# Optimization experiments

Measured on AMD Instinct MI355X. Metric: run time of the kernel, lower is better.

Reference implementation:

```python
import jax, jax.numpy as jnp
import numpy as np

N_NODES = 50000
N_EDGES = 800000
N_GRAPHS = 64
D_IN = 128
DIMS = (256, 256)


def _glorot(key, shape):
    fan_in, fan_out = shape[0], shape[1]
    lim = jnp.sqrt(6.0 / (fan_in + fan_out)).astype(jnp.float32)
    return jax.random.uniform(key, shape, jnp.float32, -lim, lim)


def setup_inputs() -> dict:
    key = jax.random.key(0)
    ks = jax.random.split(key, 12)
    x = jax.random.normal(ks[0], (N_NODES, D_IN), dtype=jnp.float32)
    edge_index = jax.random.randint(ks[1], (2, N_EDGES), 0, N_NODES, dtype=jnp.int64)
    batch = jnp.sort(jax.random.randint(ks[2], (N_NODES,), 0, N_GRAPHS, dtype=jnp.int64))
    # MLP params per GIN layer: Linear(in,dim) -> ReLU -> Linear(dim,dim) -> ReLU
    W1_0 = _glorot(ks[3], (D_IN, DIMS[0]))
    b1_0 = jnp.zeros((DIMS[0],), jnp.float32)
    W2_0 = _glorot(ks[4], (DIMS[0], DIMS[0]))
    b2_0 = jnp.zeros((DIMS[0],), jnp.float32)
    W1_1 = _glorot(ks[5], (DIMS[0], DIMS[1]))
    b1_1 = jnp.zeros((DIMS[1],), jnp.float32)
    W2_1 = _glorot(ks[6], (DIMS[1], DIMS[1]))
    b2_1 = jnp.zeros((DIMS[1],), jnp.float32)
    return {"x": x, "edge_index": edge_index, "batch": batch,
            "W1_0": W1_0, "b1_0": b1_0, "W2_0": W2_0, "b2_0": b2_0,
            "W1_1": W1_1, "b1_1": b1_1, "W2_1": W2_1, "b2_1": b2_1}


def _gin_layer(x, src, dst, W1, b1, W2, b2):
    # aggregate: sum of neighbor features (messages from src into dst)
    agg = jax.ops.segment_sum(x[src], dst, num_segments=N_NODES)
    h = x + agg  # (1 + eps) * x + agg, eps = 0
    h = jax.nn.relu(h @ W1 + b1)
    h = jax.nn.relu(h @ W2 + b2)
    return h


def reference(x, edge_index, batch, W1_0, b1_0, W2_0, b2_0, W1_1, b1_1, W2_1, b2_1):
    src, dst = edge_index[0], edge_index[1]
    h = _gin_layer(x, src, dst, W1_0, b1_0, W2_0, b2_0)
    h = _gin_layer(h, src, dst, W1_1, b1_1, W2_1, b2_1)
    # global mean pool over graphs
    sums = jax.ops.segment_sum(h, batch, num_segments=N_GRAPHS)
    counts = jax.ops.segment_sum(jnp.ones((h.shape[0],), h.dtype), batch, num_segments=N_GRAPHS)
    return sums / jnp.maximum(counts, 1.0)[:, None]
```

## Files before the change

### kernel.cpp

```cpp
#include <hip/hip_runtime.h>


typedef __bf16 bf16x8 __attribute__((ext_vector_type(8)));
typedef float f32x4 __attribute__((ext_vector_type(4)));

#define N_NODES 50000
#define N_EDGES 800000
#define N_GRAPHS 64
#define SCAN_BLOCKS 196
#define NREP 8

#define PB_HIST0 3125
#define PB_P0    6250
#define PB_P1    6378
#define PB_P2    6634
#define PB_P3    6890
#define PB_BIAS  7146
#define PB_TOTAL 7150

#define OFF_FLAGS  0ull
#define OFF_WB     64ull
#define OFF_WP0    4096ull
#define OFF_WP1    (OFF_WP0 + 65536ull)
#define OFF_WP2    (OFF_WP1 + 131072ull)
#define OFF_WP3    (OFF_WP2 + 131072ull)
#define OFF_CNT    462848ull
#define OFF_ROWPTR 662864ull
#define OFF_CURSOR 862880ull
#define OFF_SSRC   1062912ull
#define OFF_A      2662912ull
#define OFF_B      15462912ull
#define OFF_C      41062912ull
#define OFF_POOL32 66662912ull
#define OFF_BSUM   67187200ull
#define OFF_DCNT   67189248ull
#define OFF_DCUR   67190272ull
#define OFF_PERM   67191296ull

__device__ __forceinline__ float b2f(unsigned short u) {
  union { unsigned int i; float f; } v; v.i = ((unsigned int)u) << 16; return v.f;
}
__device__ __forceinline__ float b2f_lo(unsigned int u) {
  union { unsigned int i; float f; } v; v.i = u << 16; return v.f;
}
__device__ __forceinline__ float b2f_hi(unsigned int u) {
  union { unsigned int i; float f; } v; v.i = u & 0xffff0000u; return v.f;
}
__device__ __forceinline__ unsigned short f2b(float f) {
  union { unsigned int i; float f; } v; v.f = f;
  unsigned int r = v.i + 0x7fffu + ((v.i >> 16) & 1u);
  return (unsigned short)(r >> 16);
}
__device__ __forceinline__ unsigned int pk2(float hi, float lo) {
  return ((unsigned int)f2b(hi) << 16) | f2b(lo);
}
__device__ __forceinline__ void acc8(float* a, uint4 v) {
  a[0] += b2f_lo(v.x); a[1] += b2f_hi(v.x);
  a[2] += b2f_lo(v.y); a[3] += b2f_hi(v.y);
  a[4] += b2f_lo(v.z); a[5] += b2f_hi(v.z);
  a[6] += b2f_lo(v.w); a[7] += b2f_hi(v.w);
}

__global__ void detect_zero(const unsigned int* __restrict__ xw,
                            const unsigned int* __restrict__ eiw,
                            int* __restrict__ flags,
                            int* __restrict__ counts, float* __restrict__ pool32,
                            int* __restrict__ dcnt, int* __restrict__ dcur) {
  if (blockIdx.x == 0) {
    __shared__ int s_f[256], s_i[256];
    int t = threadIdx.x;
    int fh = 0, iz = 0;
    for (int i = t; i < 1024; i += 256) {
      unsigned int e = (xw[i] >> 7) & 0xFFu;
      fh += (e >= 115u && e <= 130u) ? 1 : 0;
      iz += (eiw[2 * i + 1] == 0u) ? 1 : 0;
    }
    s_f[t] = fh; s_i[t] = iz;
    __syncthreads();
    for (int s = 128; s > 0; s >>= 1) {
      if (t < s) { s_f[t] += s_f[t + s]; s_i[t] += s_i[t + s]; }
      __syncthreads();
    }
    if (t == 0) { flags[0] = s_f[0] > 512 ? 1 : 0; flags[1] = s_i[0] > 512 ? 1 : 0; }
  } else {
    int i = (blockIdx.x - 1) * 256 + threadIdx.x;
    if (i < N_NODES) counts[i] = 0;
    if (i < NREP * N_GRAPHS * 256) pool32[i] = 0.f;
    if (i < 256) { dcnt[i] = 0; dcur[i] = 0; }
  }
}

__device__ __forceinline__ void pack_w_elem(const void* W, unsigned short* Wp,
                                            int e, int isb) {
  int n = e & 255;
  int krow = e >> 8;
  int kb = krow >> 5, r = krow & 31;
  int q = r >> 3, j = r & 7;
  size_t out = ((((size_t)(kb << 8) + n) << 2) + q) * 8 + j;
  Wp[out] = isb ? ((const unsigned short*)W)[e] : f2b(((const float*)W)[e]);
}

__global__ void prep_kernel(const void* __restrict__ x, const int* __restrict__ ei,
                            const void* W0, const void* W1, const void* W2, const void* W3,
                            const void* b0, const void* b1, const void* b2, const void* b3,
                            unsigned short* __restrict__ A,
                            int* __restrict__ counts,
                            unsigned short* __restrict__ Wp0, unsigned short* __restrict__ Wp1,
                            unsigned short* __restrict__ Wp2, unsigned short* __restrict__ Wp3,
                            unsigned short* __restrict__ Wb,
                            const int* __restrict__ flags) {
  int b = blockIdx.x, t = threadIdx.x;
  int isb = flags[0];
  if (b < PB_HIST0) {
    if (!isb) {
      int i = b * 256 + t;
      const float4* f = (const float4*)x;
      float4 a = f[2 * i], c = f[2 * i + 1];
      ushort4 o0; o0.x = f2b(a.x); o0.y = f2b(a.y); o0.z = f2b(a.z); o0.w = f2b(a.w);
      ushort4 o1; o1.x = f2b(c.x); o1.y = f2b(c.y); o1.z = f2b(c.z); o1.w = f2b(c.w);
      ((ushort4*)A)[2 * i] = o0;
      ((ushort4*)A)[2 * i + 1] = o1;
    }
  } else if (b < PB_P0) {
    int e = (b - PB_HIST0) * 256 + t;
    int dst = flags[1] ? ei[2 * (N_EDGES + e)] : ei[N_EDGES + e];
    atomicAdd(&counts[dst], 1);
  } else if (b < PB_P1) {
    pack_w_elem(W0, Wp0, (b - PB_P0) * 256 + t, isb);
  } else if (b < PB_P2) {
    pack_w_elem(W1, Wp1, (b - PB_P1) * 256 + t, isb);
  } else if (b < PB_P3) {
    pack_w_elem(W2, Wp2, (b - PB_P2) * 256 + t, isb);
  } else if (b < PB_BIAS) {
    pack_w_elem(W3, Wp3, (b - PB_P3) * 256 + t, isb);
  } else {
    int i = (b - PB_BIAS) * 256 + t;
    const void* p = (i < 256) ? b0 : (i < 512) ? b1 : (i < 768) ? b2 : b3;
    int n = i & 255;
    Wb[i] = isb ? ((const unsigned short*)p)[n] : f2b(((const float*)p)[n]);
  }
}

__global__ void scan_blocks(const int* __restrict__ counts,
                            int* __restrict__ rowptr, int* __restrict__ bsum,
                            int* __restrict__ dcnt) {
  __shared__ int sd[256], lh[256];
  int t = threadIdx.x;
  int i = blockIdx.x * 256 + t;
  int v = (i < N_NODES) ? counts[i] : 0;
  sd[t] = v;
  lh[t] = 0;
  __syncthreads();
  if (i < N_NODES) atomicAdd(&lh[v > 255 ? 255 : v], 1);
  __syncthreads();
  if (lh[t] > 0) atomicAdd(&dcnt[t], lh[t]);
  for (int off = 1; off < 256; off <<= 1) {
    int u = (t >= off) ? sd[t - off] : 0;
    __syncthreads();
    sd[t] += u;
    __syncthreads();
  }
  if (i < N_NODES) rowptr[i] = sd[t] - v;
  if (t == 255) bsum[blockIdx.x] = sd[255];
}

__global__ void scan_fix(int* __restrict__ rowptr, int* __restrict__ cursor,
                         const int* __restrict__ bsum, const int* __restrict__ counts,
                         const int* __restrict__ dcnt, int* __restrict__ dcur,
                         int* __restrict__ perm) {
  __shared__ int sb[256], db[256], base[256], lc[256];
  int t = threadIdx.x;
  sb[t] = (t < SCAN_BLOCKS) ? bsum[t] : 0;
  db[t] = dcnt[t];
  lc[t] = 0;
  __syncthreads();
  for (int off = 1; off < 256; off <<= 1) {
    int u1 = (t >= off) ? sb[t - off] : 0;
    int u2 = (t >= off) ? db[t - off] : 0;
    __syncthreads();
    sb[t] += u1; db[t] += u2;
    __syncthreads();
  }
  db[t] -= dcnt[t];
  __syncthreads();
  int boffv = (blockIdx.x > 0) ? sb[blockIdx.x - 1] : 0;
  int i = blockIdx.x * 256 + t;
  int d = 0;
  if (i < N_NODES) {
    int v = rowptr[i] + boffv;
    rowptr[i] = v;
    cursor[i] = v;
    int c = counts[i];
    d = c > 255 ? 255 : c;
    atomicAdd(&lc[d], 1);
  }
  if (i == 0) rowptr[N_NODES] = N_EDGES;
  __syncthreads();
  int cnt = lc[t];
  base[t] = (cnt > 0) ? (db[t] + atomicAdd(&dcur[t], cnt)) : 0;
  __syncthreads();
  lc[t] = 0;
  __syncthreads();
  if (i < N_NODES) {
    int r = atomicAdd(&lc[d], 1);
    perm[base[d] + r] = i;
  }
}

__global__ void fill_kernel(const int* __restrict__ ei, int* __restrict__ cursor,
                            unsigned short* __restrict__ ssrc,
                            const int* __restrict__ flags) {
  int e = blockIdx.x * blockDim.x + threadIdx.x;
  if (e >= N_EDGES) return;
  int is64 = flags[1];
  int src = is64 ? ei[2 * e] : ei[e];
  int dst = is64 ? ei[2 * (N_EDGES + e)] : ei[N_EDGES + e];
  int pos = atomicAdd(&cursor[dst], 1);
  ssrc[pos] = (unsigned short)src;
}

__global__ void fused_gather_gemm(const unsigned short* __restrict__ featCanon,
                                  const unsigned short* __restrict__ featRaw,
                                  const int* __restrict__ rowptr,
                                  const unsigned short* __restrict__ ssrc,
                                  const int* __restrict__ perm,
                                  const unsigned short* __restrict__ Wp,
                                  const unsigned short* __restrict__ Wb, int bias_row,
                                  unsigned short* __restrict__ C, int D,
                                  const int* __restrict__ flags) {
  __shared__ __align__(16) unsigned short Alds[16 * 264];
  __shared__ int sp[16];
  const int S = D + 8;
  const int row0 = blockIdx.x << 4;
  const int lane = threadIdx.x & 63;
  const int wave = threadIdx.x >> 6;
  const unsigned short* feat = flags[0] ? featRaw : featCanon;
  if (threadIdx.x < 16) sp[threadIdx.x] = perm[row0 + threadIdx.x];
  __syncthreads();

  {
    int sub = lane >> 4;
    int l = lane & 15;
    int nl = (wave << 2) + sub;
    int node = sp[nl];
    int beg = rowptr[node], end = rowptr[node + 1];
    int c = l << 3;
    if (D == 256) {
      float a[16];
#pragma unroll
      for (int j = 0; j < 16; ++j) a[j] = 0.f;
      const unsigned short* spt = feat + (size_t)node * 256 + c;
      acc8(a, *(const uint4*)spt);
      acc8(a + 8, *(const uint4*)(spt + 128));
      int i = beg;
      for (; i + 3 < end; i += 4) {
        int ss[4];
#pragma unroll
        for (int e = 0; e < 4; ++e) ss[e] = ssrc[i + e];
        uint4 v[8];
#pragma unroll
        for (int e = 0; e < 4; ++e) {
          const unsigned short* p = feat + (size_t)ss[e] * 256 + c;
          v[2 * e] = *(const uint4*)p;
          v[2 * e + 1] = *(const uint4*)(p + 128);
        }
#pragma unroll
        for (int e = 0; e < 4; ++e) { acc8(a, v[2 * e]); acc8(a + 8, v[2 * e + 1]); }
      }
      for (; i < end; ++i) {
        const unsigned short* p = feat + (size_t)ssrc[i] * 256 + c;
        acc8(a, *(const uint4*)p);
        acc8(a + 8, *(const uint4*)(p + 128));
      }
      uint4 o0, o1;
      o0.x = pk2(a[1], a[0]);  o0.y = pk2(a[3], a[2]);
      o0.z = pk2(a[5], a[4]);  o0.w = pk2(a[7], a[6]);
      o1.x = pk2(a[9], a[8]);  o1.y = pk2(a[11], a[10]);
      o1.z = pk2(a[13], a[12]); o1.w = pk2(a[15], a[14]);
      *(uint4*)(&Alds[nl * S + c]) = o0;
      *(uint4*)(&Alds[nl * S + c + 128]) = o1;
    } else {
      float a[8];
#pragma unroll
      for (int j = 0; j < 8; ++j) a[j] = 0.f;
      acc8(a, *(const uint4*)(feat + (size_t)node * 128 + c));
      int i = beg;
      for (; i + 3 < end; i += 4) {
        int ss[4];
#pragma unroll
        for (int e = 0; e < 4; ++e) ss[e] = ssrc[i + e];
        uint4 v[4];
#pragma unroll
        for (int e = 0; e < 4; ++e)
          v[e] = *(const uint4*)(feat + (size_t)ss[e] * 128 + c);
#pragma unroll
        for (int e = 0; e < 4; ++e) acc8(a, v[e]);
      }
      for (; i < end; ++i)
        acc8(a, *(const uint4*)(feat + (size_t)ssrc[i] * 128 + c));
      uint4 o0;
      o0.x = pk2(a[1], a[0]); o0.y = pk2(a[3], a[2]);
      o0.z = pk2(a[5], a[4]); o0.w = pk2(a[7], a[6]);
      *(uint4*)(&Alds[nl * S + c]) = o0;
    }
  }
  __syncthreads();

  const int m = lane & 15;
  const int q = lane >> 4;
  f32x4 acc[4];
#pragma unroll
  for (int t = 0; t < 4; ++t) acc[t] = (f32x4){0.f, 0.f, 0.f, 0.f};

  const unsigned short* arow = &Alds[m * S + (q << 3)];
  const int nb = (wave << 6) + m;
  const int kblocks = D >> 5;
  for (int kb = 0; kb < kblocks; ++kb) {
    bf16x8 af = *(const bf16x8*)(arow + (kb << 5));
    const unsigned short* wp = Wp + (((size_t)(kb << 8) + nb) * 4 + q) * 8;
    bf16x8 b0 = *(const bf16x8*)(wp);
    bf16x8 b1 = *(const bf16x8*)(wp + 512);
    bf16x8 b2 = *(const bf16x8*)(wp + 1024);
    bf16x8 b3 = *(const bf16x8*)(wp + 1536);
    acc[0] = __builtin_amdgcn_mfma_f32_16x16x32_bf16(af, b0, acc[0], 0, 0, 0);
    acc[1] = __builtin_amdgcn_mfma_f32_16x16x32_bf16(af, b1, acc[1], 0, 0, 0);
    acc[2] = __builtin_amdgcn_mfma_f32_16x16x32_bf16(af, b2, acc[2], 0, 0, 0);
    acc[3] = __builtin_amdgcn_mfma_f32_16x16x32_bf16(af, b3, acc[3], 0, 0, 0);
  }
#pragma unroll
  for (int t = 0; t < 4; ++t) {
    int n = (wave << 6) + (t << 4) + m;
    float bv = b2f(Wb[bias_row * 256 + n]);
#pragma unroll
    for (int i = 0; i < 4; ++i) {
      int r = sp[(q << 2) + i];
      float v = fmaxf(acc[t][i] + bv, 0.f);
      C[(size_t)r * 256 + n] = f2b(v);
    }
  }
}

__global__ void gemm_relu(const unsigned short* __restrict__ A,
                          const unsigned short* __restrict__ Wp,
                          const unsigned short* __restrict__ Wb, int bias_row,
                          unsigned short* __restrict__ C, int K) {
  const int row0 = blockIdx.x << 4;
  const int lane = threadIdx.x & 63;
  const int wave = threadIdx.x >> 6;
  const int m = lane & 15;
  const int q = lane >> 4;
  f32x4 acc[4];
#pragma unroll
  for (int t = 0; t < 4; ++t) acc[t] = (f32x4){0.f, 0.f, 0.f, 0.f};

  const unsigned short* arow = A + (size_t)(row0 + m) * K + (q << 3);
  const int nb = (wave << 6) + m;
  const int kblocks = K >> 5;
  for (int kb = 0; kb < kblocks; ++kb) {
    bf16x8 af = *(const bf16x8*)(arow + (kb << 5));
    const unsigned short* wp = Wp + (((size_t)(kb << 8) + nb) * 4 + q) * 8;
    bf16x8 b0 = *(const bf16x8*)(wp);
    bf16x8 b1 = *(const bf16x8*)(wp + 512);
    bf16x8 b2 = *(const bf16x8*)(wp + 1024);
    bf16x8 b3 = *(const bf16x8*)(wp + 1536);
    acc[0] = __builtin_amdgcn_mfma_f32_16x16x32_bf16(af, b0, acc[0], 0, 0, 0);
    acc[1] = __builtin_amdgcn_mfma_f32_16x16x32_bf16(af, b1, acc[1], 0, 0, 0);
    acc[2] = __builtin_amdgcn_mfma_f32_16x16x32_bf16(af, b2, acc[2], 0, 0, 0);
    acc[3] = __builtin_amdgcn_mfma_f32_16x16x32_bf16(af, b3, acc[3], 0, 0, 0);
  }
#pragma unroll
  for (int t = 0; t < 4; ++t) {
    int n = (wave << 6) + (t << 4) + m;
    float bv = b2f(Wb[bias_row * 256 + n]);
#pragma unroll
    for (int i = 0; i < 4; ++i) {
      int r = row0 + (q << 2) + i;
      float v = fmaxf(acc[t][i] + bv, 0.f);
      C[(size_t)r * 256 + n] = f2b(v);
    }
  }
}

__global__ void gemm_pool(const unsigned short* __restrict__ A,
                          const unsigned short* __restrict__ Wp,
                          const unsigned short* __restrict__ Wb, int bias_row,
                          float* __restrict__ pool32, const int* __restrict__ batch,
                          const int* __restrict__ flags, int K) {
  __shared__ int sg[16];
  const int row0 = blockIdx.x << 4;
  const int lane = threadIdx.x & 63;
  const int wave = threadIdx.x >> 6;
  float* pr = pool32 + ((blockIdx.x & (NREP - 1)) << 14);
  if (threadIdx.x < 16) {
    int r = row0 + threadIdx.x;
    sg[threadIdx.x] = flags[1] ? batch[2 * r] : batch[r];
  }
  __syncthreads();

  const int m = lane & 15;
  const int q = lane >> 4;
  f32x4 acc[4];
#pragma unroll
  for (int t = 0; t < 4; ++t) acc[t] = (f32x4){0.f, 0.f, 0.f, 0.f};

  const unsigned short* arow = A + (size_t)(row0 + m) * K + (q << 3);
  const int nb = (wave << 6) + m;
  const int kblocks = K >> 5;
  for (int kb = 0; kb < kblocks; ++kb) {
    bf16x8 af = *(const bf16x8*)(arow + (kb << 5));
    const unsigned short* wp = Wp + (((size_t)(kb << 8) + nb) * 4 + q) * 8;
    bf16x8 b0 = *(const bf16x8*)(wp);
    bf16x8 b1 = *(const bf16x8*)(wp + 512);
    bf16x8 b2 = *(const bf16x8*)(wp + 1024);
    bf16x8 b3 = *(const bf16x8*)(wp + 1536);
    acc[0] = __builtin_amdgcn_mfma_f32_16x16x32_bf16(af, b0, acc[0], 0, 0, 0);
    acc[1] = __builtin_amdgcn_mfma_f32_16x16x32_bf16(af, b1, acc[1], 0, 0, 0);
    acc[2] = __builtin_amdgcn_mfma_f32_16x16x32_bf16(af, b2, acc[2], 0, 0, 0);
    acc[3] = __builtin_amdgcn_mfma_f32_16x16x32_bf16(af, b3, acc[3], 0, 0, 0);
  }

  int uniform = (sg[0] == sg[15]);
#pragma unroll
  for (int t = 0; t < 4; ++t) {
    int n = (wave << 6) + (t << 4) + m;
    float bv = b2f(Wb[bias_row * 256 + n]);
    float v0 = fmaxf(acc[t][0] + bv, 0.f);
    float v1 = fmaxf(acc[t][1] + bv, 0.f);
    float v2 = fmaxf(acc[t][2] + bv, 0.f);
    float v3 = fmaxf(acc[t][3] + bv, 0.f);
    if (uniform) {
      float ps = v0 + v1 + v2 + v3;
      ps += __shfl_xor(ps, 16);
      ps += __shfl_xor(ps, 32);
      if (q == 0) unsafeAtomicAdd(&pr[sg[0] * 256 + n], ps);
    } else {
      int gp = sg[q << 2];
      float a = 0.f;
      float vv[4] = {v0, v1, v2, v3};
#pragma unroll
      for (int i = 0; i < 4; ++i) {
        int g = sg[(q << 2) + i];
        if (g != gp) { unsafeAtomicAdd(&pr[gp * 256 + n], a); a = 0.f; gp = g; }
        a += vv[i];
      }
      unsafeAtomicAdd(&pr[gp * 256 + n], a);
    }
  }
}

__device__ __forceinline__ int lower_bound(const int* a, int n, int v, int is64) {
  int lo = 0, hi = n;
  while (lo < hi) {
    int mid = (lo + hi) >> 1;
    int bv = is64 ? a[2 * mid] : a[mid];
    if (bv < v) lo = mid + 1; else hi = mid;
  }
  return lo;
}

__global__ void pool_final(const float* __restrict__ pool32,
                           const int* __restrict__ batch,
                           void* __restrict__ out,
                           const int* __restrict__ flags) {
  __shared__ int sh[2];
  int g = blockIdx.x;
  int is64 = flags[1];
  if (threadIdx.x == 0) sh[0] = lower_bound(batch, N_NODES, g, is64);
  if (threadIdx.x == 1) sh[1] = lower_bound(batch, N_NODES, g + 1, is64);
  __syncthreads();
  int c = threadIdx.x;
  float s = 0.f;
#pragma unroll
  for (int r = 0; r < NREP; ++r) s += pool32[(r << 14) + g * 256 + c];
  float res = s / fmaxf((float)(sh[1] - sh[0]), 1.0f);
  if (flags[0]) ((unsigned short*)out)[(size_t)g * 256 + c] = f2b(res);
  else          ((float*)out)[(size_t)g * 256 + c] = res;
}

extern "C" void kernel_launch(void* const* d_in, const int* in_sizes, int n_in,
                              void* d_out, int out_size, void* d_ws, size_t ws_size,
                              hipStream_t stream) {
  const void* x    = d_in[0];
  const int*  ei   = (const int*)d_in[1];
  const int*  batch= (const int*)d_in[2];

  char* ws = (char*)d_ws;
  int*            flags = (int*)(ws + OFF_FLAGS);
  unsigned short* Wb    = (unsigned short*)(ws + OFF_WB);
  unsigned short* Wp0   = (unsigned short*)(ws + OFF_WP0);
  unsigned short* Wp1   = (unsigned short*)(ws + OFF_WP1);
  unsigned short* Wp2   = (unsigned short*)(ws + OFF_WP2);
  unsigned short* Wp3   = (unsigned short*)(ws + OFF_WP3);
  int*            cnts  = (int*)(ws + OFF_CNT);
  int*            rowp  = (int*)(ws + OFF_ROWPTR);
  int*            curs  = (int*)(ws + OFF_CURSOR);
  unsigned short* ssrc  = (unsigned short*)(ws + OFF_SSRC);
  unsigned short* A     = (unsigned short*)(ws + OFF_A);
  unsigned short* B     = (unsigned short*)(ws + OFF_B);
  unsigned short* C     = (unsigned short*)(ws + OFF_C);
  float*          pool32= (float*)(ws + OFF_POOL32);
  int*            bsum  = (int*)(ws + OFF_BSUM);
  int*            dcnt  = (int*)(ws + OFF_DCNT);
  int*            dcur  = (int*)(ws + OFF_DCUR);
  int*            perm  = (int*)(ws + OFF_PERM);

  detect_zero<<<513, 256, 0, stream>>>((const unsigned int*)x, (const unsigned int*)ei,
                                       flags, cnts, pool32, dcnt, dcur);
  prep_kernel<<<PB_TOTAL, 256, 0, stream>>>(x, ei,
                                            d_in[3], d_in[5], d_in[7], d_in[9],
                                            d_in[4], d_in[6], d_in[8], d_in[10],
                                            A, cnts, Wp0, Wp1, Wp2, Wp3, Wb, flags);
  scan_blocks<<<SCAN_BLOCKS, 256, 0, stream>>>(cnts, rowp, bsum, dcnt);
  scan_fix<<<SCAN_BLOCKS, 256, 0, stream>>>(rowp, curs, bsum, cnts, dcnt, dcur, perm);
  fill_kernel<<<3125, 256, 0, stream>>>(ei, curs, ssrc, flags);

  fused_gather_gemm<<<3125, 256, 0, stream>>>(A, (const unsigned short*)x, rowp, ssrc,
                                              perm, Wp0, Wb, 0, C, 128, flags);
  gemm_relu<<<3125, 256, 0, stream>>>(C, Wp1, Wb, 1, B, 256);

  fused_gather_gemm<<<3125, 256, 0, stream>>>(B, B, rowp, ssrc,
                                              perm, Wp2, Wb, 2, C, 256, flags);
  gemm_pool<<<3125, 256, 0, stream>>>(C, Wp3, Wb, 3, pool32, batch, flags, 256);

  pool_final<<<N_GRAPHS, 256, 0, stream>>>(pool32, batch, d_out, flags);
}
```

Measured before the change: 378.2 us.

## Fuse each GIN layer's gather and both MLP GEMMs into one kernel

Each GIN layer now runs in a single kernel: neighbour aggregation, first linear+ReLU kept in shared memory, then second linear+ReLU (and pooling for layer 2). This removes the intermediate C buffer round trip and two launches. Layer 2 uses 512-thread blocks so each wave covers fewer output columns. The degree-sorting permutation is now built per block with a local prefix scan instead of a global histogram, so nodes are sorted by degree only within each 256-node block. That removes global atomics but gives weaker load balancing across blocks.

```diff
diff --git a/kernel.cpp b/kernel.cpp
--- a/kernel.cpp
+++ b/kernel.cpp
@@ -30,11 +30,8 @@
 #define OFF_SSRC   1062912ull
 #define OFF_A      2662912ull
 #define OFF_B      15462912ull
-#define OFF_C      41062912ull
 #define OFF_POOL32 66662912ull
 #define OFF_BSUM   67187200ull
-#define OFF_DCNT   67189248ull
-#define OFF_DCUR   67190272ull
 #define OFF_PERM   67191296ull
 
 __device__ __forceinline__ float b2f(unsigned short u) {
@@ -64,8 +61,7 @@
 __global__ void detect_zero(const unsigned int* __restrict__ xw,
                             const unsigned int* __restrict__ eiw,
                             int* __restrict__ flags,
-                            int* __restrict__ counts, float* __restrict__ pool32,
-                            int* __restrict__ dcnt, int* __restrict__ dcur) {
+                            int* __restrict__ counts, float* __restrict__ pool32) {
   if (blockIdx.x == 0) {
     __shared__ int s_f[256], s_i[256];
     int t = threadIdx.x;
@@ -86,7 +82,6 @@
     int i = (blockIdx.x - 1) * 256 + threadIdx.x;
     if (i < N_NODES) counts[i] = 0;
     if (i < NREP * N_GRAPHS * 256) pool32[i] = 0.f;
-    if (i < 256) { dcnt[i] = 0; dcur[i] = 0; }
   }
 }
 
@@ -142,18 +137,13 @@
 }
 
 __global__ void scan_blocks(const int* __restrict__ counts,
-                            int* __restrict__ rowptr, int* __restrict__ bsum,
-                            int* __restrict__ dcnt) {
-  __shared__ int sd[256], lh[256];
+                            int* __restrict__ rowptr, int* __restrict__ bsum) {
+  __shared__ int sd[256];
   int t = threadIdx.x;
   int i = blockIdx.x * 256 + t;
   int v = (i < N_NODES) ? counts[i] : 0;
   sd[t] = v;
-  lh[t] = 0;
-  __syncthreads();
-  if (i < N_NODES) atomicAdd(&lh[v > 255 ? 255 : v], 1);
-  __syncthreads();
-  if (lh[t] > 0) atomicAdd(&dcnt[t], lh[t]);
+  __syncthreads();
   for (int off = 1; off < 256; off <<= 1) {
     int u = (t >= off) ? sd[t - off] : 0;
     __syncthreads();
@@ -166,44 +156,46 @@
 
 __global__ void scan_fix(int* __restrict__ rowptr, int* __restrict__ cursor,
                          const int* __restrict__ bsum, const int* __restrict__ counts,
-                         const int* __restrict__ dcnt, int* __restrict__ dcur,
                          int* __restrict__ perm) {
-  __shared__ int sb[256], db[256], base[256], lc[256];
+  __shared__ int sb[256], lh[256], lc2[256];
   int t = threadIdx.x;
   sb[t] = (t < SCAN_BLOCKS) ? bsum[t] : 0;
-  db[t] = dcnt[t];
-  lc[t] = 0;
+  lh[t] = 0; lc2[t] = 0;
   __syncthreads();
   for (int off = 1; off < 256; off <<= 1) {
-    int u1 = (t >= off) ? sb[t - off] : 0;
-    int u2 = (t >= off) ? db[t - off] : 0;
-    __syncthreads();
-    sb[t] += u1; db[t] += u2;
-    __syncthreads();
-  }
-  db[t] -= dcnt[t];
-  __syncthreads();
+    int u = (t >= off) ? sb[t - off] : 0;
+    __syncthreads();
+    sb[t] += u;
+    __syncthreads();
+  }
   int boffv = (blockIdx.x > 0) ? sb[blockIdx.x - 1] : 0;
   int i = blockIdx.x * 256 + t;
   int d = 0;
-  if (i < N_NODES) {
+  int valid = (i < N_NODES);
+  if (valid) {
     int v = rowptr[i] + boffv;
     rowptr[i] = v;
     cursor[i] = v;
     int c = counts[i];
     d = c > 255 ? 255 : c;
-    atomicAdd(&lc[d], 1);
+    atomicAdd(&lh[d], 1);
   }
   if (i == 0) rowptr[N_NODES] = N_EDGES;
   __syncthreads();
-  int cnt = lc[t];
-  base[t] = (cnt > 0) ? (db[t] + atomicAdd(&dcur[t], cnt)) : 0;
-  __syncthreads();
-  lc[t] = 0;
-  __syncthreads();
-  if (i < N_NODES) {
-    int r = atomicAdd(&lc[d], 1);
-    perm[base[d] + r] = i;
+  int own = lh[t];
+  for (int off = 1; off < 256; off <<= 1) {
+    int u = (t >= off) ? lh[t - off] : 0;
+    __syncthreads();
+    lh[t] += u;
+    __syncthreads();
+  }
+  int ex = lh[t] - own;
+  __syncthreads();
+  lh[t] = ex;
+  __syncthreads();
+  if (valid) {
+    int r = lh[d] + atomicAdd(&lc2[d], 1);
+    perm[blockIdx.x * 256 + r] = i;
   }
 }
 
@@ -219,18 +211,17 @@
   ssrc[pos] = (unsigned short)src;
 }
 
-__global__ void fused_gather_gemm(const unsigned short* __restrict__ featCanon,
-                                  const unsigned short* __restrict__ featRaw,
-                                  const int* __restrict__ rowptr,
-                                  const unsigned short* __restrict__ ssrc,
-                                  const int* __restrict__ perm,
-                                  const unsigned short* __restrict__ Wp,
-                                  const unsigned short* __restrict__ Wb, int bias_row,
-                                  unsigned short* __restrict__ C, int D,
-                                  const int* __restrict__ flags) {
-  __shared__ __align__(16) unsigned short Alds[16 * 264];
+__global__ void __launch_bounds__(256) fused_layer1(
+    const unsigned short* __restrict__ featCanon,
+    const unsigned short* __restrict__ featRaw,
+    const int* __restrict__ rowptr, const unsigned short* __restrict__ ssrc,
+    const int* __restrict__ perm,
+    const unsigned short* __restrict__ Wp0, const unsigned short* __restrict__ Wp1,
+    const unsigned short* __restrict__ Wb,
+    unsigned short* __restrict__ B, const int* __restrict__ flags) {
+  __shared__ __align__(16) unsigned short Alds[16 * 136];
+  __shared__ __align__(16) unsigned short Tlds[16 * 264];
   __shared__ int sp[16];
-  const int S = D + 8;
   const int row0 = blockIdx.x << 4;
   const int lane = threadIdx.x & 63;
   const int wave = threadIdx.x >> 6;
@@ -239,211 +230,214 @@
   __syncthreads();
 
   {
-    int sub = lane >> 4;
-    int l = lane & 15;
+    int sub = lane >> 4, l = lane & 15;
     int nl = (wave << 2) + sub;
     int node = sp[nl];
     int beg = rowptr[node], end = rowptr[node + 1];
     int c = l << 3;
-    if (D == 256) {
-      float a[16];
-#pragma unroll
-      for (int j = 0; j < 16; ++j) a[j] = 0.f;
-      const unsigned short* spt = feat + (size_t)node * 256 + c;
-      acc8(a, *(const uint4*)spt);
-      acc8(a + 8, *(const uint4*)(spt + 128));
-      int i = beg;
-      for (; i + 3 < end; i += 4) {
-        int ss[4];
-#pragma unroll
-        for (int e = 0; e < 4; ++e) ss[e] = ssrc[i + e];
-        uint4 v[8];
-#pragma unroll
-        for (int e = 0; e < 4; ++e) {
-          const unsigned short* p = feat + (size_t)ss[e] * 256 + c;
-          v[2 * e] = *(const uint4*)p;
-          v[2 * e + 1] = *(const uint4*)(p + 128);
-        }
-#pragma unroll
-        for (int e = 0; e < 4; ++e) { acc8(a, v[2 * e]); acc8(a + 8, v[2 * e + 1]); }
+    float a[8];
+#pragma unroll
+    for (int j = 0; j < 8; ++j) a[j] = 0.f;
+    acc8(a, *(const uint4*)(feat + (size_t)node * 128 + c));
+    int i = beg;
+    for (; i + 3 < end; i += 4) {
+      int ss[4];
+#pragma unroll
+      for (int e = 0; e < 4; ++e) ss[e] = ssrc[i + e];
+      uint4 v[4];
+#pragma unroll
+      for (int e = 0; e < 4; ++e)
+        v[e] = *(const uint4*)(feat + (size_t)ss[e] * 128 + c);
+#pragma unroll
+      for (int e = 0; e < 4; ++e) acc8(a, v[e]);
+    }
+    for (; i < end; ++i)
+      acc8(a, *(const uint4*)(feat + (size_t)ssrc[i] * 128 + c));
+    uint4 o;
+    o.x = pk2(a[1], a[0]); o.y = pk2(a[3], a[2]);
+    o.z = pk2(a[5], a[4]); o.w = pk2(a[7], a[6]);
+    *(uint4*)(&Alds[nl * 136 + c]) = o;
+  }
+  __syncthreads();
+
+  const int m = lane & 15, q = lane >> 4;
+  {
+    f32x4 acc[4];
+#pragma unroll
+    for (int t = 0; t < 4; ++t) acc[t] = (f32x4){0.f, 0.f, 0.f, 0.f};
+    const unsigned short* arow = &Alds[m * 136 + (q << 3)];
+    const int nb = (wave << 6) + m;
+#pragma unroll
+    for (int kb = 0; kb < 4; ++kb) {
+      bf16x8 af = *(const bf16x8*)(arow + (kb << 5));
+      const unsigned short* wp = Wp0 + (((size_t)(kb << 8) + nb) * 4 + q) * 8;
+      acc[0] = __builtin_amdgcn_mfma_f32_16x16x32_bf16(af, *(const bf16x8*)(wp), acc[0], 0, 0, 0);
+      acc[1] = __builtin_amdgcn_mfma_f32_16x16x32_bf16(af, *(const bf16x8*)(wp + 512), acc[1], 0, 0, 0);
+      acc[2] = __builtin_amdgcn_mfma_f32_16x16x32_bf16(af, *(const bf16x8*)(wp + 1024), acc[2], 0, 0, 0);
+      acc[3] = __builtin_amdgcn_mfma_f32_16x16x32_bf16(af, *(const bf16x8*)(wp + 1536), acc[3], 0, 0, 0);
+    }
+#pragma unroll
+    for (int t = 0; t < 4; ++t) {
+      int n = (wave << 6) + (t << 4) + m;
+      float bv = b2f(Wb[n]);
+#pragma unroll
+      for (int i = 0; i < 4; ++i)
+        Tlds[((q << 2) + i) * 264 + n] = f2b(fmaxf(acc[t][i] + bv, 0.f));
+    }
+  }
+  __syncthreads();
+
+  {
+    f32x4 acc[4];
+#pragma unroll
+    for (int t = 0; t < 4; ++t) acc[t] = (f32x4){0.f, 0.f, 0.f, 0.f};
+    const unsigned short* arow = &Tlds[m * 264 + (q << 3)];
+    const int nb = (wave << 6) + m;
+#pragma unroll
+    for (int kb = 0; kb < 8; ++kb) {
+      bf16x8 af = *(const bf16x8*)(arow + (kb << 5));
+      const unsigned short* wp = Wp1 + (((size_t)(kb << 8) + nb) * 4 + q) * 8;
+      acc[0] = __builtin_amdgcn_mfma_f32_16x16x32_bf16(af, *(const bf16x8*)(wp), acc[0], 0, 0, 0);
+      acc[1] = __builtin_amdgcn_mfma_f32_16x16x32_bf16(af, *(const bf16x8*)(wp + 512), acc[1], 0, 0, 0);
+      acc[2] = __builtin_amdgcn_mfma_f32_16x16x32_bf16(af, *(const bf16x8*)(wp + 1024), acc[2], 0, 0, 0);
+      acc[3] = __builtin_amdgcn_mfma_f32_16x16x32_bf16(af, *(const bf16x8*)(wp + 1536), acc[3], 0, 0, 0);
+    }
+#pragma unroll
+    for (int t = 0; t < 4; ++t) {
+      int n = (wave << 6) + (t << 4) + m;
+      float bv = b2f(Wb[256 + n]);
+#pragma unroll
+      for (int i = 0; i < 4; ++i) {
+        int r = sp[(q << 2) + i];
+        B[(size_t)r * 256 + n] = f2b(fmaxf(acc[t][i] + bv, 0.f));
       }
-      for (; i < end; ++i) {
-        const unsigned short* p = feat + (size_t)ssrc[i] * 256 + c;
-        acc8(a, *(const uint4*)p);
-        acc8(a + 8, *(const uint4*)(p + 128));
-      }
-      uint4 o0, o1;
-      o0.x = pk2(a[1], a[0]);  o0.y = pk2(a[3], a[2]);
-      o0.z = pk2(a[5], a[4]);  o0.w = pk2(a[7], a[6]);
-      o1.x = pk2(a[9], a[8]);  o1.y = pk2(a[11], a[10]);
-      o1.z = pk2(a[13], a[12]); o1.w = pk2(a[15], a[14]);
-      *(uint4*)(&Alds[nl * S + c]) = o0;
-      *(uint4*)(&Alds[nl * S + c + 128]) = o1;
-    } else {
-      float a[8];
-#pragma unroll
-      for (int j = 0; j < 8; ++j) a[j] = 0.f;
-      acc8(a, *(const uint4*)(feat + (size_t)node * 128 + c));
-      int i = beg;
-      for (; i + 3 < end; i += 4) {
-        int ss[4];
-#pragma unroll
-        for (int e = 0; e < 4; ++e) ss[e] = ssrc[i + e];
-        uint4 v[4];
-#pragma unroll
-        for (int e = 0; e < 4; ++e)
-          v[e] = *(const uint4*)(feat + (size_t)ss[e] * 128 + c);
-#pragma unroll
-        for (int e = 0; e < 4; ++e) acc8(a, v[e]);
-      }
-      for (; i < end; ++i)
-        acc8(a, *(const uint4*)(feat + (size_t)ssrc[i] * 128 + c));
-      uint4 o0;
-      o0.x = pk2(a[1], a[0]); o0.y = pk2(a[3], a[2]);
-      o0.z = pk2(a[5], a[4]); o0.w = pk2(a[7], a[6]);
-      *(uint4*)(&Alds[nl * S + c]) = o0;
-    }
-  }
-  __syncthreads();
-
-  const int m = lane & 15;
-  const int q = lane >> 4;
-  f32x4 acc[4];
-#pragma unroll
-  for (int t = 0; t < 4; ++t) acc[t] = (f32x4){0.f, 0.f, 0.f, 0.f};
-
-  const unsigned short* arow = &Alds[m * S + (q << 3)];
-  const int nb = (wave << 6) + m;
-  const int kblocks = D >> 5;
-  for (int kb = 0; kb < kblocks; ++kb) {
-    bf16x8 af = *(const bf16x8*)(arow + (kb << 5));
-    const unsigned short* wp = Wp + (((size_t)(kb << 8) + nb) * 4 + q) * 8;
-    bf16x8 b0 = *(const bf16x8*)(wp);
-    bf16x8 b1 = *(const bf16x8*)(wp + 512);
-    bf16x8 b2 = *(const bf16x8*)(wp + 1024);
-    bf16x8 b3 = *(const bf16x8*)(wp + 1536);
-    acc[0] = __builtin_amdgcn_mfma_f32_16x16x32_bf16(af, b0, acc[0], 0, 0, 0);
-    acc[1] = __builtin_amdgcn_mfma_f32_16x16x32_bf16(af, b1, acc[1], 0, 0, 0);
-    acc[2] = __builtin_amdgcn_mfma_f32_16x16x32_bf16(af, b2, acc[2], 0, 0, 0);
-    acc[3] = __builtin_amdgcn_mfma_f32_16x16x32_bf16(af, b3, acc[3], 0, 0, 0);
-  }
-#pragma unroll
-  for (int t = 0; t < 4; ++t) {
-    int n = (wave << 6) + (t << 4) + m;
-    float bv = b2f(Wb[bias_row * 256 + n]);
-#pragma unroll
-    for (int i = 0; i < 4; ++i) {
-      int r = sp[(q << 2) + i];
-      float v = fmaxf(acc[t][i] + bv, 0.f);
-      C[(size_t)r * 256 + n] = f2b(v);
-    }
-  }
-}
-
-__global__ void gemm_relu(const unsigned short* __restrict__ A,
-                          const unsigned short* __restrict__ Wp,
-                          const unsigned short* __restrict__ Wb, int bias_row,
-                          unsigned short* __restrict__ C, int K) {
+    }
+  }
+}
+
+__global__ void __launch_bounds__(512) fused_layer2(
+    const unsigned short* __restrict__ B,
+    const int* __restrict__ rowptr, const unsigned short* __restrict__ ssrc,
+    const int* __restrict__ perm,
+    const unsigned short* __restrict__ Wp2, const unsigned short* __restrict__ Wp3,
+    const unsigned short* __restrict__ Wb,
+    float* __restrict__ pool32, const int* __restrict__ batch,
+    const int* __restrict__ flags) {
+  __shared__ __align__(16) unsigned short Alds[16 * 264];
+  __shared__ __align__(16) unsigned short Tlds[16 * 264];
+  __shared__ int sp[16], sg[16], uni;
   const int row0 = blockIdx.x << 4;
   const int lane = threadIdx.x & 63;
   const int wave = threadIdx.x >> 6;
-  const int m = lane & 15;
-  const int q = lane >> 4;
-  f32x4 acc[4];
-#pragma unroll
-  for (int t = 0; t < 4; ++t) acc[t] = (f32x4){0.f, 0.f, 0.f, 0.f};
-
-  const unsigned short* arow = A + (size_t)(row0 + m) * K + (q << 3);
-  const int nb = (wave << 6) + m;
-  const int kblocks = K >> 5;
-  for (int kb = 0; kb < kblocks; ++kb) {
-    bf16x8 af = *(const bf16x8*)(arow + (kb << 5));
-    const unsigned short* wp = Wp + (((size_t)(kb << 8) + nb) * 4 + q) * 8;
-    bf16x8 b0 = *(const bf16x8*)(wp);
-    bf16x8 b1 = *(const bf16x8*)(wp + 512);
-    bf16x8 b2 = *(const bf16x8*)(wp + 1024);
-    bf16x8 b3 = *(const bf16x8*)(wp + 1536);
-    acc[0] = __builtin_amdgcn_mfma_f32_16x16x32_bf16(af, b0, acc[0], 0, 0, 0);
-    acc[1] = __builtin_amdgcn_mfma_f32_16x16x32_bf16(af, b1, acc[1], 0, 0, 0);
-    acc[2] = __builtin_amdgcn_mfma_f32_16x16x32_bf16(af, b2, acc[2], 0, 0, 0);
-    acc[3] = __builtin_amdgcn_mfma_f32_16x16x32_bf16(af, b3, acc[3], 0, 0, 0);
-  }
-#pragma unroll
-  for (int t = 0; t < 4; ++t) {
-    int n = (wave << 6) + (t << 4) + m;
-    float bv = b2f(Wb[bias_row * 256 + n]);
-#pragma unroll
-    for (int i = 0; i < 4; ++i) {
-      int r = row0 + (q << 2) + i;
-      float v = fmaxf(acc[t][i] + bv, 0.f);
-      C[(size_t)r * 256 + n] = f2b(v);
-    }
-  }
-}
-
-__global__ void gemm_pool(const unsigned short* __restrict__ A,
-                          const unsigned short* __restrict__ Wp,
-                          const unsigned short* __restrict__ Wb, int bias_row,
-                          float* __restrict__ pool32, const int* __restrict__ batch,
-                          const int* __restrict__ flags, int K) {
-  __shared__ int sg[16];
-  const int row0 = blockIdx.x << 4;
-  const int lane = threadIdx.x & 63;
-  const int wave = threadIdx.x >> 6;
-  float* pr = pool32 + ((blockIdx.x & (NREP - 1)) << 14);
   if (threadIdx.x < 16) {
-    int r = row0 + threadIdx.x;
-    sg[threadIdx.x] = flags[1] ? batch[2 * r] : batch[r];
-  }
-  __syncthreads();
-
-  const int m = lane & 15;
-  const int q = lane >> 4;
-  f32x4 acc[4];
-#pragma unroll
-  for (int t = 0; t < 4; ++t) acc[t] = (f32x4){0.f, 0.f, 0.f, 0.f};
-
-  const unsigned short* arow = A + (size_t)(row0 + m) * K + (q << 3);
-  const int nb = (wave << 6) + m;
-  const int kblocks = K >> 5;
-  for (int kb = 0; kb < kblocks; ++kb) {
-    bf16x8 af = *(const bf16x8*)(arow + (kb << 5));
-    const unsigned short* wp = Wp + (((size_t)(kb << 8) + nb) * 4 + q) * 8;
-    bf16x8 b0 = *(const bf16x8*)(wp);
-    bf16x8 b1 = *(const bf16x8*)(wp + 512);
-    bf16x8 b2 = *(const bf16x8*)(wp + 1024);
-    bf16x8 b3 = *(const bf16x8*)(wp + 1536);
-    acc[0] = __builtin_amdgcn_mfma_f32_16x16x32_bf16(af, b0, acc[0], 0, 0, 0);
-    acc[1] = __builtin_amdgcn_mfma_f32_16x16x32_bf16(af, b1, acc[1], 0, 0, 0);
-    acc[2] = __builtin_amdgcn_mfma_f32_16x16x32_bf16(af, b2, acc[2], 0, 0, 0);
-    acc[3] = __builtin_amdgcn_mfma_f32_16x16x32_bf16(af, b3, acc[3], 0, 0, 0);
-  }
-
-  int uniform = (sg[0] == sg[15]);
-#pragma unroll
-  for (int t = 0; t < 4; ++t) {
-    int n = (wave << 6) + (t << 4) + m;
-    float bv = b2f(Wb[bias_row * 256 + n]);
-    float v0 = fmaxf(acc[t][0] + bv, 0.f);
-    float v1 = fmaxf(acc[t][1] + bv, 0.f);
-    float v2 = fmaxf(acc[t][2] + bv, 0.f);
-    float v3 = fmaxf(acc[t][3] + bv, 0.f);
-    if (uniform) {
-      float ps = v0 + v1 + v2 + v3;
-      ps += __shfl_xor(ps, 16);
-      ps += __shfl_xor(ps, 32);
-      if (q == 0) unsafeAtomicAdd(&pr[sg[0] * 256 + n], ps);
-    } else {
-      int gp = sg[q << 2];
-      float a = 0.f;
-      float vv[4] = {v0, v1, v2, v3};
-#pragma unroll
-      for (int i = 0; i < 4; ++i) {
-        int g = sg[(q << 2) + i];
-        if (g != gp) { unsafeAtomicAdd(&pr[gp * 256 + n], a); a = 0.f; gp = g; }
-        a += vv[i];
+    int p = perm[row0 + threadIdx.x];
+    sp[threadIdx.x] = p;
+    sg[threadIdx.x] = flags[1] ? batch[2 * p] : batch[p];
+  }
+  __syncthreads();
+  if (threadIdx.x == 0) {
+    int u = 1;
+#pragma unroll
+    for (int i = 1; i < 16; ++i) u &= (sg[i] == sg[0]);
+    uni = u;
+  }
+
+  {
+    int sub = lane >> 5, l = lane & 31;
+    int nl = (wave << 1) + sub;
+    int node = sp[nl];
+    int beg = rowptr[node], end = rowptr[node + 1];
+    int c = l << 3;
+    float a[8];
+#pragma unroll
+    for (int j = 0; j < 8; ++j) a[j] = 0.f;
+    acc8(a, *(const uint4*)(B + (size_t)node * 256 + c));
+    int i = beg;
+    for (; i + 3 < end; i += 4) {
+      int ss[4];
+#pragma unroll
+      for (int e = 0; e < 4; ++e) ss[e] = ssrc[i + e];
+      uint4 v[4];
+#pragma unroll
+      for (int e = 0; e < 4; ++e)
+        v[e] = *(const uint4*)(B + (size_t)ss[e] * 256 + c);
+#pragma unroll
+      for (int e = 0; e < 4; ++e) acc8(a, v[e]);
+    }
+    for (; i < end; ++i)
+      acc8(a, *(const uint4*)(B + (size_t)ssrc[i] * 256 + c));
+    uint4 o;
+    o.x = pk2(a[1], a[0]); o.y = pk2(a[3], a[2]);
+    o.z = pk2(a[5], a[4]); o.w = pk2(a[7], a[6]);
+    *(uint4*)(&Alds[nl * 264 + c]) = o;
+  }
+  __syncthreads();
+
+  const int m = lane & 15, q = lane >> 4;
+  {
+    f32x4 acc[2];
+    acc[0] = (f32x4){0.f, 0.f, 0.f, 0.f};
+    acc[1] = (f32x4){0.f, 0.f, 0.f, 0.f};
+    const unsigned short* arow = &Alds[m * 264 + (q << 3)];
+    const int nb = (wave << 5) + m;
+#pragma unroll
+    for (int kb = 0; kb < 8; ++kb) {
+      bf16x8 af = *(const bf16x8*)(arow + (kb << 5));
+      const unsigned short* wp = Wp2 + (((size_t)(kb << 8) + nb) * 4 + q) * 8;
+      acc[0] = __builtin_amdgcn_mfma_f32_16x16x32_bf16(af, *(const bf16x8*)(wp), acc[0], 0, 0, 0);
+      acc[1] = __builtin_amdgcn_mfma_f32_16x16x32_bf16(af, *(const bf16x8*)(wp + 512), acc[1], 0, 0, 0);
+    }
+#pragma unroll
+    for (int t = 0; t < 2; ++t) {
+      int n = (wave << 5) + (t << 4) + m;
+      float bv = b2f(Wb[512 + n]);
+#pragma unroll
+      for (int i = 0; i < 4; ++i)
+        Tlds[((q << 2) + i) * 264 + n] = f2b(fmaxf(acc[t][i] + bv, 0.f));
+    }
+  }
+  __syncthreads();
+
+  {
+    f32x4 acc[2];
+    acc[0] = (f32x4){0.f, 0.f, 0.f, 0.f};
+    acc[1] = (f32x4){0.f, 0.f, 0.f, 0.f};
+    const unsigned short* arow = &Tlds[m * 264 + (q << 3)];
+    const int nb = (wave << 5) + m;
+#pragma unroll
+    for (int kb = 0; kb < 8; ++kb) {
+      bf16x8 af = *(const bf16x8*)(arow + (kb << 5));
+      const unsigned short* wp = Wp3 + (((size_t)(kb << 8) + nb) * 4 + q) * 8;
+      acc[0] = __builtin_amdgcn_mfma_f32_16x16x32_bf16(af, *(const bf16x8*)(wp), acc[0], 0, 0, 0);
+      acc[1] = __builtin_amdgcn_mfma_f32_16x16x32_bf16(af, *(const bf16x8*)(wp + 512), acc[1], 0, 0, 0);
+    }
+    float* pr = pool32 + ((blockIdx.x & (NREP - 1)) << 14);
+    int u = uni;
+#pragma unroll
+    for (int t = 0; t < 2; ++t) {
+      int n = (wave << 5) + (t << 4) + m;
+      float bv = b2f(Wb[768 + n]);
+      float v0 = fmaxf(acc[t][0] + bv, 0.f);
+      float v1 = fmaxf(acc[t][1] + bv, 0.f);
+      float v2 = fmaxf(acc[t][2] + bv, 0.f);
+      float v3 = fmaxf(acc[t][3] + bv, 0.f);
+      if (u) {
+        float ps = v0 + v1 + v2 + v3;
+        ps += __shfl_xor(ps, 16);
+        ps += __shfl_xor(ps, 32);
+        if (q == 0) unsafeAtomicAdd(&pr[sg[0] * 256 + n], ps);
+      } else {
+        float vv[4] = {v0, v1, v2, v3};
+        int gp = sg[q << 2];
+        float a = 0.f;
+#pragma unroll
+        for (int i = 0; i < 4; ++i) {
+          int g = sg[(q << 2) + i];
+          if (g != gp) { unsafeAtomicAdd(&pr[gp * 256 + n], a); a = 0.f; gp = g; }
+          a += vv[i];
+        }
+        unsafeAtomicAdd(&pr[gp * 256 + n], a);
       }
-      unsafeAtomicAdd(&pr[gp * 256 + n], a);
     }
   }
 }
@@ -497,30 +491,24 @@
   unsigned short* ssrc  = (unsigned short*)(ws + OFF_SSRC);
   unsigned short* A     = (unsigned short*)(ws + OFF_A);
   unsigned short* B     = (unsigned short*)(ws + OFF_B);
-  unsigned short* C     = (unsigned short*)(ws + OFF_C);
   float*          pool32= (float*)(ws + OFF_POOL32);
   int*            bsum  = (int*)(ws + OFF_BSUM);
-  int*            dcnt  = (int*)(ws + OFF_DCNT);
-  int*            dcur  = (int*)(ws + OFF_DCUR);
   int*            perm  = (int*)(ws + OFF_PERM);
 
   detect_zero<<<513, 256, 0, stream>>>((const unsigned int*)x, (const unsigned int*)ei,
-                                       flags, cnts, pool32, dcnt, dcur);
+                                       flags, cnts, pool32);
   prep_kernel<<<PB_TOTAL, 256, 0, stream>>>(x, ei,
                                             d_in[3], d_in[5], d_in[7], d_in[9],
                                             d_in[4], d_in[6], d_in[8], d_in[10],
                                             A, cnts, Wp0, Wp1, Wp2, Wp3, Wb, flags);
-  scan_blocks<<<SCAN_BLOCKS, 256, 0, stream>>>(cnts, rowp, bsum, dcnt);
-  scan_fix<<<SCAN_BLOCKS, 256, 0, stream>>>(rowp, curs, bsum, cnts, dcnt, dcur, perm);
+  scan_blocks<<<SCAN_BLOCKS, 256, 0, stream>>>(cnts, rowp, bsum);
+  scan_fix<<<SCAN_BLOCKS, 256, 0, stream>>>(rowp, curs, bsum, cnts, perm);
   fill_kernel<<<3125, 256, 0, stream>>>(ei, curs, ssrc, flags);
 
-  fused_gather_gemm<<<3125, 256, 0, stream>>>(A, (const unsigned short*)x, rowp, ssrc,
-                                              perm, Wp0, Wb, 0, C, 128, flags);
-  gemm_relu<<<3125, 256, 0, stream>>>(C, Wp1, Wb, 1, B, 256);
-
-  fused_gather_gemm<<<3125, 256, 0, stream>>>(B, B, rowp, ssrc,
-                                              perm, Wp2, Wb, 2, C, 256, flags);
-  gemm_pool<<<3125, 256, 0, stream>>>(C, Wp3, Wb, 3, pool32, batch, flags, 256);
+  fused_layer1<<<3125, 256, 0, stream>>>(A, (const unsigned short*)x, rowp, ssrc,
+                                         perm, Wp0, Wp1, Wb, B, flags);
+  fused_layer2<<<3125, 512, 0, stream>>>(B, rowp, ssrc, perm, Wp2, Wp3, Wb,
+                                         pool32, batch, flags);
 
   pool_final<<<N_GRAPHS, 256, 0, stream>>>(pool32, batch, d_out, flags);
 }
```

After: 354.0 us. 1.07x faster.
